# Kernel tuning notes

Measured on AMD Instinct MI355X. Metric: run time of the kernel, lower is better.

## Reference

```python
import jax, jax.numpy as jnp
import numpy as np

EPS = 1e-8  # smoothing_radius


def setup_inputs() -> dict:
    key = jax.random.key(0)
    ks = jax.random.split(key, 8)
    T, S, D = 2048, 1024, 3
    H, FIN, FOUT = 64, 7, 4
    return {
        "reference_length": jnp.ones((), jnp.float32),
        "source_points": jax.random.normal(ks[0], (S, D), jnp.float32),
        "target_points": jax.random.normal(ks[1], (T, D), jnp.float32),
        "source_strengths": jax.random.uniform(ks[2], (S,), jnp.float32),
        "source_area": jax.random.uniform(ks[3], (S,), jnp.float32),
        "source_normal": jax.random.normal(ks[4], (S, D), jnp.float32),
        "W1": jax.random.normal(ks[5], (FIN, H), jnp.float32) / np.sqrt(FIN),
        "b1": jnp.zeros((H,), jnp.float32),
        "W2": jax.random.normal(ks[6], (H, FOUT), jnp.float32) / np.sqrt(H),
        "b2": jnp.zeros((FOUT,), jnp.float32),
    }


def _legendre4(x):
    # First 4 Legendre polynomials P1..P4 (n_spherical_harmonics = 4)
    x2 = x * x
    p1 = x
    p2 = 0.5 * (3.0 * x2 - 1.0)
    p3 = 0.5 * (5.0 * x2 - 3.0) * x
    p4 = 0.125 * ((35.0 * x2 - 30.0) * x2 + 3.0)
    return jnp.stack([p1, p2, p3, p4], axis=-1)


def _kernel_forward(reference_length, source_points, target_points,
                    source_strengths, source_area, source_normal,
                    W1, b1, W2, b2):
    D = source_points.shape[-1]
    # Dimensionless relative positions: [T, S, D]
    r = (target_points[:, None, :] - source_points[None, :, :]) / reference_length
    r2 = jnp.sum(r * r, axis=-1) + EPS * EPS          # [T, S]
    n2 = jnp.sum(source_normal * source_normal, -1) + EPS * EPS  # [S]
    # Invariant features: source scalar, smoothed log-magnitudes, pair Legendre terms
    log_r = 0.5 * jnp.log(r2)                          # [T, S]
    log_n = 0.5 * jnp.log(n2)                          # [S]
    cos = jnp.einsum('tsd,sd->ts', r, source_normal) / jnp.sqrt(r2 * n2[None, :])
    feats = jnp.concatenate([
        jnp.broadcast_to(source_area[None, :, None], r2.shape + (1,)),
        log_r[..., None],
        jnp.broadcast_to(log_n[None, :, None], r2.shape + (1,)),
        _legendre4(cos),
    ], axis=-1)                                        # [T, S, 7]
    # MLP kernel network with tanh squashing (network_type='mlp')
    h = jax.nn.silu(feats @ W1 + b1)                   # [T, S, 64]
    out = jnp.tanh(h @ W2 + b2)                        # [T, S, 4]
    # Physical far-field decay: scalar ~ 1/r^{D-2}, vector ~ 1/r^{D-1}
    inv_r = jax.lax.rsqrt(r2)
    decay_s = inv_r ** (D - 2)
    decay_v = inv_r ** (D - 1)
    w = source_strengths[None, :]                      # [1, S]
    scalar = jnp.sum(w * decay_s * out[..., 0], axis=-1)  # [T]
    # Rotationally invariant vector reprojection: radial + 2 coeffs per non-radial vector
    r_hat = r * inv_r[..., None]
    n_hat = source_normal / jnp.sqrt(n2)[:, None]
    n_hat_b = jnp.broadcast_to(n_hat[None], r.shape)
    vec = (out[..., 1:2] * r_hat
           + out[..., 2:3] * n_hat_b
           + out[..., 3:4] * jnp.cross(r_hat, n_hat_b))  # [T, S, D]
    vector = jnp.einsum('ts,tsd->td', w * decay_v, vec)   # [T, D]
    return jnp.concatenate([scalar[:, None], vector], axis=-1)  # [T, 1+D]


def reference(reference_length, source_points, target_points, source_strengths,
              source_area, source_normal, W1, b1, W2, b2):
    return _kernel_forward(reference_length, source_points, target_points,
                           source_strengths, source_area, source_normal,
                           W1, b1, W2, b2)
```

## Files before the change

kernel.cpp:

```cpp
#include <hip/hip_runtime.h>

typedef __attribute__((ext_vector_type(4))) float f32x4;
typedef __attribute__((ext_vector_type(8))) short bf16x8;

#define EPS2 1e-16f
constexpr int PBLOCK = 256;
constexpr int BLOCK  = 256;
constexpr float LOG2E = 1.4426950408889634f;

__device__ __forceinline__ float rcpf_fast(float x){ return __builtin_amdgcn_rcpf(x); }
__device__ __forceinline__ float rsqf_fast(float x){ return __builtin_amdgcn_rsqf(x); }
__device__ __forceinline__ float exp2_fast(float x){ return __builtin_amdgcn_exp2f(x); }
__device__ __forceinline__ unsigned cvt_pk_bf16(float lo, float hi){
    unsigned d;
    asm("v_cvt_pk_bf16_f32 %0, %1, %2" : "=v"(d) : "v"(lo), "v"(hi));
    return d;
}
__device__ __forceinline__ bf16x8 as_frag(int4 v){
    union { int4 i; bf16x8 f; } u; u.i = v; return u.f;
}

__global__ void prep(const float* __restrict__ refLenP,
                     const float* __restrict__ srcP,
                     const float* __restrict__ srcN,
                     const float* __restrict__ wgtP,
                     const float* __restrict__ areaP,
                     const float* __restrict__ W1,
                     const float* __restrict__ b1,
                     const float* __restrict__ W2,
                     float* __restrict__ ws, int S)
{
    const int nSrcBlk = (S + PBLOCK - 1) / PBLOCK;
    const int bid = blockIdx.x;
    if (bid < nSrcBlk) {
        const int s = bid * PBLOCK + threadIdx.x;
        if (s < S) {
            const float invL = rcpf_fast(refLenP[0]);
            float px = srcP[s*3+0]*invL, py = srcP[s*3+1]*invL, pz = srcP[s*3+2]*invL;
            float nx = srcN[s*3+0], ny = srcN[s*3+1], nz = srcN[s*3+2];
            float n2 = fmaf(nx,nx, fmaf(ny,ny, nz*nz)) + EPS2;
            float inv_n = rsqf_fast(n2);
            float l2n = __log2f(n2);
            float4* sPA = (float4*)(ws + 384);
            float4* sNB = (float4*)(ws + 384 + 4*S);
            float*  sw  = ws + 384 + 8*S;
            sPA[s] = make_float4(px, py, pz, areaP[s]);
            sNB[s] = make_float4(nx*inv_n, ny*inv_n, nz*inv_n, l2n);
            sw[s]  = wgtP[s];
        }
    } else {
        const int t = threadIdx.x;
        unsigned* W1u = (unsigned*)ws;
        unsigned* W2u = (unsigned*)ws + 256;
        if (t < 64) {
            const int h = t;
            float v[8];
            v[0] = -LOG2E * W1[0*64 + h];
            v[1] = -0.5f  * W1[1*64 + h];
            v[2] = -0.5f  * W1[2*64 + h];
            v[3] = -LOG2E * W1[3*64 + h];
            v[4] = -LOG2E * W1[4*64 + h];
            v[5] = -LOG2E * W1[5*64 + h];
            v[6] = -LOG2E * W1[6*64 + h];
            v[7] = -LOG2E * b1[h];
            #pragma unroll
            for (int r = 0; r < 4; ++r)
                W1u[h*4 + r] = cvt_pk_bf16(v[2*r], v[2*r+1]);
        } else if (t < 192) {
            const int idx = t - 64;
            const int j = idx >> 5;
            const int hp = idx & 31;
            float a = -2.0f * W2[(2*hp  )*4 + j];
            float b = -2.0f * W2[(2*hp+1)*4 + j];
            W2u[j*32 + hp] = cvt_pk_bf16(a, b);
        }
    }
}

__global__ __launch_bounds__(BLOCK)
void bh_kernel(const float* __restrict__ refLenP,
               const float* __restrict__ tgtP,
               const float* __restrict__ b2,
               const float* __restrict__ ws,
               float* __restrict__ out,
               int S, int T)
{
    __shared__ unsigned featsL[4][64][4];
    __shared__ unsigned hvL[4][16][36];
    __shared__ f32x4   oL[4][64];
    __shared__ float   red[4][4];

    const int tid = threadIdx.x;
    const int wv  = tid >> 6;
    const int l   = tid & 63;
    const int col = l & 15;
    const int q   = l >> 4;
    const int t   = blockIdx.x;

    const unsigned* __restrict__ W1u = (const unsigned*)ws;
    const unsigned* __restrict__ W2u = (const unsigned*)ws + 256;
    const float4* __restrict__ sPA = (const float4*)(ws + 384);
    const float4* __restrict__ sNB = (const float4*)(ws + 384 + 4*S);
    const float*  __restrict__ sw  = ws + 384 + 8*S;

    int4 A1[4];
    #pragma unroll
    for (int mt = 0; mt < 4; ++mt) {
        int4 r = *(const int4*)&W1u[(mt*16 + col) * 4];
        A1[mt] = (q == 0) ? r : make_int4(0,0,0,0);
    }
    int4 A2[2];
    #pragma unroll
    for (int kt = 0; kt < 2; ++kt) {
        const int rowj = col;
        const int src = (rowj < 4) ? rowj : 0;
        int4 r = *(const int4*)&W2u[src*32 + kt*16 + q*4];
        A2[kt] = (rowj < 4) ? r : make_int4(0,0,0,0);
    }

    const float invL = rcpf_fast(refLenP[0]);
    const float tx = tgtP[t*3+0]*invL;
    const float ty = tgtP[t*3+1]*invL;
    const float tz = tgtP[t*3+2]*invL;
    const float s2 = 2.0f * LOG2E;
    const f32x4 b2init = { s2*b2[0], s2*b2[1], s2*b2[2], s2*b2[3] };
    const f32x4 zero4  = { 0.f, 0.f, 0.f, 0.f };

    float acc0 = 0.f, acc1 = 0.f, acc2 = 0.f, acc3 = 0.f;

    for (int it = 0; it < 4; ++it) {
        const int s  = wv*256 + it*64 + l;
        const int sc = (s < S) ? s : 0;
        const float4 pa = sPA[sc];
        const float4 nb = sNB[sc];
        const float wgt = (s < S) ? sw[sc] : 0.f;

        float rx = tx - pa.x, ry = ty - pa.y, rz = tz - pa.z;
        float r2 = fmaf(rx,rx, fmaf(ry,ry, fmaf(rz,rz, EPS2)));
        float ir = rsqf_fast(r2);
        float l2r = __log2f(r2);
        float cosv = fmaf(rx,nb.x, fmaf(ry,nb.y, rz*nb.z)) * ir;
        float c2 = cosv * cosv;
        float P2 = fmaf(c2, 1.5f, -0.5f);
        float P3 = (c2*2.5f - 1.5f) * cosv;
        float P4 = fmaf(fmaf(c2, 4.375f, -3.75f), c2, 0.375f);
        unsigned f01 = cvt_pk_bf16(pa.w, l2r);
        unsigned f23 = cvt_pk_bf16(nb.w, cosv);
        unsigned f45 = cvt_pk_bf16(P2,   P3);
        unsigned f67 = cvt_pk_bf16(P4,   1.0f);
        *(int4*)&featsL[wv][l][0] = make_int4((int)f01, (int)f23, (int)f45, (int)f67);

        #pragma unroll
        for (int pb = 0; pb < 4; ++pb) {
            int4 braw = *(const int4*)&featsL[wv][pb*16 + col][0];
            int4 b1i = (q == 0) ? braw : make_int4(0,0,0,0);
            bf16x8 B1 = as_frag(b1i);

            #pragma unroll
            for (int mt = 0; mt < 4; ++mt) {
                f32x4 c1 = __builtin_amdgcn_mfma_f32_16x16x32_bf16(
                               as_frag(A1[mt]), B1, zero4, 0, 0, 0);
                float hv0, hv1, hv2, hv3;
                { float e = exp2_fast(c1[0]); hv0 = c1[0] * rcpf_fast(1.0f + e); }
                { float e = exp2_fast(c1[1]); hv1 = c1[1] * rcpf_fast(1.0f + e); }
                { float e = exp2_fast(c1[2]); hv2 = c1[2] * rcpf_fast(1.0f + e); }
                { float e = exp2_fast(c1[3]); hv3 = c1[3] * rcpf_fast(1.0f + e); }
                unsigned h01 = cvt_pk_bf16(hv0, hv1);
                unsigned h23 = cvt_pk_bf16(hv2, hv3);
                *(uint2*)&hvL[wv][col][mt*8 + q*2] = make_uint2(h01, h23);
            }

            f32x4 oacc = b2init;
            #pragma unroll
            for (int kt = 0; kt < 2; ++kt) {
                int4 b2raw = *(const int4*)&hvL[wv][col][kt*16 + q*4];
                oacc = __builtin_amdgcn_mfma_f32_16x16x32_bf16(
                           as_frag(A2[kt]), as_frag(b2raw), oacc, 0, 0, 0);
            }
            if (q == 0) oL[wv][pb*16 + col] = oacc;
        }

        f32x4 ov = oL[wv][l];
        float tt[4];
        #pragma unroll
        for (int k = 0; k < 4; ++k) {
            float m = fminf(fmaxf(ov[k], -126.f), 126.f);
            float E = exp2_fast(m);
            tt[k] = (E - 1.0f) * rcpf_fast(E + 1.0f);
        }
        float wsv = wgt * ir;
        float wvv = wsv * ir;
        acc0 = fmaf(wsv, tt[0], acc0);
        float rhx = rx*ir, rhy = ry*ir, rhz = rz*ir;
        float cxx = rhy*nb.z - rhz*nb.y;
        float cxy = rhz*nb.x - rhx*nb.z;
        float cxz = rhx*nb.y - rhy*nb.x;
        float vx = tt[1]*rhx + tt[2]*nb.x + tt[3]*cxx;
        float vy = tt[1]*rhy + tt[2]*nb.y + tt[3]*cxy;
        float vz = tt[1]*rhz + tt[2]*nb.z + tt[3]*cxz;
        acc1 = fmaf(wvv, vx, acc1);
        acc2 = fmaf(wvv, vy, acc2);
        acc3 = fmaf(wvv, vz, acc3);
    }

    #pragma unroll
    for (int off = 32; off > 0; off >>= 1) {
        acc0 += __shfl_down(acc0, off);
        acc1 += __shfl_down(acc1, off);
        acc2 += __shfl_down(acc2, off);
        acc3 += __shfl_down(acc3, off);
    }
    if ((tid & 63) == 0) {
        red[wv][0] = acc0; red[wv][1] = acc1;
        red[wv][2] = acc2; red[wv][3] = acc3;
    }
    __syncthreads();
    if (tid < 4) {
        float v = red[0][tid] + red[1][tid] + red[2][tid] + red[3][tid];
        out[t*4 + tid] = v;
    }
}

extern "C" void kernel_launch(void* const* d_in, const int* in_sizes, int n_in,
                              void* d_out, int out_size, void* d_ws, size_t ws_size,
                              hipStream_t stream) {
    const float* refLen = (const float*)d_in[0];
    const float* srcP   = (const float*)d_in[1];
    const float* tgtP   = (const float*)d_in[2];
    const float* w      = (const float*)d_in[3];
    const float* area   = (const float*)d_in[4];
    const float* srcN   = (const float*)d_in[5];
    const float* W1     = (const float*)d_in[6];
    const float* b1     = (const float*)d_in[7];
    const float* W2     = (const float*)d_in[8];
    const float* b2     = (const float*)d_in[9];
    float* out          = (float*)d_out;
    float* ws           = (float*)d_ws;

    const int S = in_sizes[3];
    const int T = in_sizes[2] / 3;
    const int nSrcBlk = (S + PBLOCK - 1) / PBLOCK;

    prep<<<nSrcBlk + 1, PBLOCK, 0, stream>>>(refLen, srcP, srcN, w, area, W1, b1, W2, ws, S);
    bh_kernel<<<T, BLOCK, 0, stream>>>(refLen, tgtP, b2, ws, out, S, T);
}
```

Before: 110.2 us.

## Keep MFMA fragments in registers via permuted W2 layout and lane shuffles

```diff
diff --git a/kernel.cpp b/kernel.cpp
--- a/kernel.cpp
+++ b/kernel.cpp
@@ -69,10 +69,14 @@
         } else if (t < 192) {
             const int idx = t - 64;
             const int j = idx >> 5;
-            const int hp = idx & 31;
-            float a = -2.0f * W2[(2*hp  )*4 + j];
-            float b = -2.0f * W2[(2*hp+1)*4 + j];
-            W2u[j*32 + hp] = cvt_pk_bf16(a, b);
+            const int u = idx & 31;
+            const int kt = u >> 4;
+            const int q  = (u >> 2) & 3;
+            const int w  = u & 3;
+            const int m = 32*kt + (w>>1)*16 + 4*q + (w&1)*2;
+            float a = -2.0f * W2[ m      * 4 + j];
+            float b = -2.0f * W2[(m + 1) * 4 + j];
+            W2u[j*32 + u] = cvt_pk_bf16(a, b);
         }
     }
 }
@@ -85,10 +89,7 @@
                float* __restrict__ out,
                int S, int T)
 {
-    __shared__ unsigned featsL[4][64][4];
-    __shared__ unsigned hvL[4][16][36];
-    __shared__ f32x4   oL[4][64];
-    __shared__ float   red[4][4];
+    __shared__ float red[4][4];
 
     const int tid = threadIdx.x;
     const int wv  = tid >> 6;
@@ -144,18 +145,21 @@
         float P2 = fmaf(c2, 1.5f, -0.5f);
         float P3 = (c2*2.5f - 1.5f) * cosv;
         float P4 = fmaf(fmaf(c2, 4.375f, -3.75f), c2, 0.375f);
-        unsigned f01 = cvt_pk_bf16(pa.w, l2r);
-        unsigned f23 = cvt_pk_bf16(nb.w, cosv);
-        unsigned f45 = cvt_pk_bf16(P2,   P3);
-        unsigned f67 = cvt_pk_bf16(P4,   1.0f);
-        *(int4*)&featsL[wv][l][0] = make_int4((int)f01, (int)f23, (int)f45, (int)f67);
+        unsigned fp0 = cvt_pk_bf16(pa.w, l2r);
+        unsigned fp1 = cvt_pk_bf16(nb.w, cosv);
+        unsigned fp2 = cvt_pk_bf16(P2,   P3);
+        unsigned fp3 = cvt_pk_bf16(P4,   1.0f);
+
+        f32x4 ov = zero4;
 
         #pragma unroll
         for (int pb = 0; pb < 4; ++pb) {
-            int4 braw = *(const int4*)&featsL[wv][pb*16 + col][0];
-            int4 b1i = (q == 0) ? braw : make_int4(0,0,0,0);
+            const int srcl = pb*16 + col;
+            int4 b1i = make_int4((int)__shfl(fp0, srcl), (int)__shfl(fp1, srcl),
+                                 (int)__shfl(fp2, srcl), (int)__shfl(fp3, srcl));
             bf16x8 B1 = as_frag(b1i);
 
+            unsigned pk[4][2];
             #pragma unroll
             for (int mt = 0; mt < 4; ++mt) {
                 f32x4 c1 = __builtin_amdgcn_mfma_f32_16x16x32_bf16(
@@ -165,26 +169,27 @@
                 { float e = exp2_fast(c1[1]); hv1 = c1[1] * rcpf_fast(1.0f + e); }
                 { float e = exp2_fast(c1[2]); hv2 = c1[2] * rcpf_fast(1.0f + e); }
                 { float e = exp2_fast(c1[3]); hv3 = c1[3] * rcpf_fast(1.0f + e); }
-                unsigned h01 = cvt_pk_bf16(hv0, hv1);
-                unsigned h23 = cvt_pk_bf16(hv2, hv3);
-                *(uint2*)&hvL[wv][col][mt*8 + q*2] = make_uint2(h01, h23);
+                pk[mt][0] = cvt_pk_bf16(hv0, hv1);
+                pk[mt][1] = cvt_pk_bf16(hv2, hv3);
             }
 
+            int4 B2a = make_int4((int)pk[0][0], (int)pk[0][1], (int)pk[1][0], (int)pk[1][1]);
+            int4 B2b = make_int4((int)pk[2][0], (int)pk[2][1], (int)pk[3][0], (int)pk[3][1]);
             f32x4 oacc = b2init;
+            oacc = __builtin_amdgcn_mfma_f32_16x16x32_bf16(as_frag(A2[0]), as_frag(B2a), oacc, 0, 0, 0);
+            oacc = __builtin_amdgcn_mfma_f32_16x16x32_bf16(as_frag(A2[1]), as_frag(B2b), oacc, 0, 0, 0);
+
             #pragma unroll
-            for (int kt = 0; kt < 2; ++kt) {
-                int4 b2raw = *(const int4*)&hvL[wv][col][kt*16 + q*4];
-                oacc = __builtin_amdgcn_mfma_f32_16x16x32_bf16(
-                           as_frag(A2[kt]), as_frag(b2raw), oacc, 0, 0, 0);
+            for (int k = 0; k < 4; ++k) {
+                float tmp = __shfl(oacc[k], col);
+                ov[k] = (q == pb) ? tmp : ov[k];
             }
-            if (q == 0) oL[wv][pb*16 + col] = oacc;
-        }
-
-        f32x4 ov = oL[wv][l];
+        }
+
         float tt[4];
         #pragma unroll
         for (int k = 0; k < 4; ++k) {
-            float m = fminf(fmaxf(ov[k], -126.f), 126.f);
+            float m = __builtin_amdgcn_fmed3f(ov[k], -126.f, 126.f);
             float E = exp2_fast(m);
             tt[k] = (E - 1.0f) * rcpf_fast(E + 1.0f);
         }
```

Result: no change. 110.5 us (+0.3%).
